# Kernel tuning notes

Hardware: AMD Instinct MI355X
Metric: run time of the kernel (lower is better)

Reference implementation:

```python
import jax, jax.numpy as jnp
import numpy as np

B, H, W, C = 16, 32, 32, 256
N = H * W


def setup_inputs() -> dict:
    key = jax.random.key(0)
    ks = jax.random.split(key, 8)
    x = jax.random.normal(ks[0], (B, H, W, C), dtype=jnp.float32)
    # nn.LazyLinear(C): weight (C, C), bias (C,)
    scale = 1.0 / np.sqrt(C)
    Wq = jax.random.uniform(ks[1], (C, C), jnp.float32, -scale, scale)
    bq = jax.random.uniform(ks[2], (C,), jnp.float32, -scale, scale)
    Wk = jax.random.uniform(ks[3], (C, C), jnp.float32, -scale, scale)
    bk = jax.random.uniform(ks[4], (C,), jnp.float32, -scale, scale)
    Wv = jax.random.uniform(ks[5], (C, C), jnp.float32, -scale, scale)
    bv = jax.random.uniform(ks[6], (C,), jnp.float32, -scale, scale)
    # torch.randn(H, H*W, W)
    Wp = jax.random.normal(ks[7], (H, N, W), dtype=jnp.float32)
    return {"x": x, "Wq": Wq, "bq": bq, "Wk": Wk, "bk": bk,
            "Wv": Wv, "bv": bv, "Wp": Wp}


def reference(x, Wq, bq, Wk, bk, Wv, bv, Wp):
    b, h, w, c = x.shape
    n = h * w
    # Linear projections (torch Linear: x @ W^T + b), flatten spatial dims to N tokens
    q = (jnp.einsum('bhwc,dc->bhwd', x, Wq) + bq).reshape(b, n, c)
    k = (jnp.einsum('bhwc,dc->bhwd', x, Wk) + bk).reshape(b, n, c)
    v = (jnp.einsum('bhwc,dc->bhwd', x, Wv) + bv).reshape(b, n, c)
    # Unscaled attention over the N spatial tokens (no 1/sqrt(C) in the original)
    scores = jnp.einsum('bnc,bmc->bnm', q, k)          # (B, N, N)
    attn = jax.nn.softmax(scores, axis=-1)
    qkv = jnp.einsum('bnm,bmc->bnc', attn, v)           # (B, N, C)
    # z = (qkv^T [B,1,C,N] @ Wp [H,N,W]).transpose(-2,-1) -> (B, H, W, C)
    z = jnp.einsum('bnc,hnw->bhwc', qkv, Wp)
    return z
```

## Files before the change

### kernel.cpp

```cpp
#include <hip/hip_runtime.h>
#include <hip/hip_bf16.h>

#define BB 16
#define NN 1024
#define CC 256

typedef __attribute__((ext_vector_type(8))) short bf16x8;
typedef __attribute__((ext_vector_type(4))) float f32x4;

#define GPTR(p) ((const __attribute__((address_space(1))) void*)(p))
#define LPTR(p) ((__attribute__((address_space(3))) void*)(p))

__device__ __forceinline__ unsigned short f2bf(float f) {
  union { float f; unsigned u; } v; v.f = f;
  unsigned r = v.u + 0x7FFFu + ((v.u >> 16) & 1u);
  return (unsigned short)(r >> 16);
}

__global__ void cast_all(const float* __restrict__ x,
                         const float* __restrict__ Wq, const float* __restrict__ Wk,
                         const float* __restrict__ Wv,
                         const float* __restrict__ bq, const float* __restrict__ bk,
                         const float* __restrict__ bv,
                         unsigned short* __restrict__ xb,
                         unsigned short* __restrict__ wqkvb,
                         float* __restrict__ bqkv) {
  const int NX = BB * NN * CC;
  const int NW = CC * CC;
  int i = blockIdx.x * blockDim.x + threadIdx.x;
  if (i < NX) { xb[i] = f2bf(x[i]); return; }
  int j = i - NX;
  if (j < 3 * NW) {
    const float* w = (j < NW) ? Wq : (j < 2 * NW ? Wk : Wv);
    wqkvb[j] = f2bf(w[j % NW]);
    return;
  }
  int jj = j - 3 * NW;
  if (jj < 3 * CC) {
    const float* bb = (jj < CC) ? bq : (jj < 2 * CC ? bk : bv);
    bqkv[jj] = bb[jj % CC];
  }
}

__global__ __launch_bounds__(256) void wp_transpose(const float* __restrict__ Wp,
                                                    unsigned short* __restrict__ Amat) {
  __shared__ float tile[32][33];
  int h = blockIdx.y;
  int n0 = blockIdx.x * 32;
#pragma unroll
  for (int j = 0; j < 4; j++) {
    int idx = threadIdx.x + j * 256;
    int a = idx >> 5, wc = idx & 31;
    tile[a][wc] = Wp[(size_t)h * (NN * 32) + (size_t)(n0 + a) * 32 + wc];
  }
  __syncthreads();
#pragma unroll
  for (int j = 0; j < 4; j++) {
    int idx = threadIdx.x + j * 256;
    int wc = idx >> 5, a = idx & 31;
    Amat[(size_t)(h * 32 + wc) * NN + n0 + a] = f2bf(tile[a][wc]);
  }
}

template <int BIAS_MODE, int F32OUT>
__global__ __launch_bounds__(256) void gemm_tile(
    const unsigned short* __restrict__ A, int lda, long sA,
    const unsigned short* __restrict__ Bt, int ldb, long sB,
    const float* __restrict__ bias,
    void* __restrict__ Out, int ldo, long sO, int K) {
  __shared__ unsigned short As[2 * 128 * 32];
  __shared__ unsigned short Bs[2 * 64 * 32];
  int b = blockIdx.x;
  int m0 = blockIdx.y * 128;
  int n0 = blockIdx.z * 64;
  int t = threadIdx.x;
  int w = t >> 6, lane = t & 63;
  int wm = (w >> 1) * 64, wn = (w & 1) * 32;
  int r = lane & 15, g = lane >> 4;

  const unsigned short* Ab = A + (long)b * sA;
  const unsigned short* Bb = Bt + (long)b * sB;

  int srow = t >> 2;
  int scol = (t & 3) * 8;

  f32x4 acc[4][2];
#pragma unroll
  for (int i = 0; i < 4; i++)
#pragma unroll
    for (int j = 0; j < 2; j++) acc[i][j] = (f32x4){0.f, 0.f, 0.f, 0.f};

  for (int k0 = 0; k0 < K; k0 += 64) {
    __syncthreads();
#pragma unroll
    for (int kh = 0; kh < 2; kh++) {
#pragma unroll
      for (int jj = 0; jj < 2; jj++) {
        __builtin_amdgcn_global_load_lds(
            GPTR(Ab + (long)(m0 + srow + jj * 64) * lda + k0 + kh * 32 + scol),
            LPTR(&As[kh * 4096 + jj * 2048 + t * 8]), 16, 0, 0);
      }
      __builtin_amdgcn_global_load_lds(
          GPTR(Bb + (long)(n0 + srow) * ldb + k0 + kh * 32 + scol),
          LPTR(&Bs[kh * 2048 + t * 8]), 16, 0, 0);
    }
    __syncthreads();
#pragma unroll
    for (int kh = 0; kh < 2; kh++) {
      bf16x8 af[4], bfr[2];
#pragma unroll
      for (int ti = 0; ti < 4; ti++)
        af[ti] = *(const bf16x8*)&As[kh * 4096 + (wm + ti * 16 + r) * 32 + g * 8];
#pragma unroll
      for (int tj = 0; tj < 2; tj++)
        bfr[tj] = *(const bf16x8*)&Bs[kh * 2048 + (wn + tj * 16 + r) * 32 + g * 8];
#pragma unroll
      for (int ti = 0; ti < 4; ti++)
#pragma unroll
        for (int tj = 0; tj < 2; tj++)
          acc[ti][tj] = __builtin_amdgcn_mfma_f32_16x16x32_bf16(af[ti], bfr[tj], acc[ti][tj], 0, 0, 0);
    }
  }

#pragma unroll
  for (int ti = 0; ti < 4; ti++) {
#pragma unroll
    for (int tj = 0; tj < 2; tj++) {
      int col = n0 + wn + tj * 16 + r;
      float bc = (BIAS_MODE == 1) ? bias[col] : 0.0f;
#pragma unroll
      for (int rr = 0; rr < 4; rr++) {
        int row = m0 + wm + ti * 16 + g * 4 + rr;
        float val = acc[ti][tj][rr] + bc;
        long oidx = (long)b * sO + (long)row * ldo + col;
        if (F32OUT)
          ((float*)Out)[oidx] = val;
        else
          ((unsigned short*)Out)[oidx] = f2bf(val);
      }
    }
  }
}

__global__ __launch_bounds__(256) void gemm_qkv(
    const unsigned short* __restrict__ A,
    const unsigned short* __restrict__ Bt,
    const float* __restrict__ bias,
    unsigned short* __restrict__ Qb, unsigned short* __restrict__ Kb,
    unsigned short* __restrict__ Vtb) {
  __shared__ unsigned short As[2 * 128 * 32];
  __shared__ unsigned short Bs[2 * 64 * 32];
  int b = blockIdx.x;
  int m0 = blockIdx.y * 128;
  int n0 = blockIdx.z * 64;
  int t = threadIdx.x;
  int w = t >> 6, lane = t & 63;
  int wm = (w >> 1) * 64, wn = (w & 1) * 32;
  int r = lane & 15, g = lane >> 4;

  const unsigned short* Ab = A + (long)b * NN * CC;
  int srow = t >> 2;
  int scol = (t & 3) * 8;

  f32x4 acc[4][2];
#pragma unroll
  for (int i = 0; i < 4; i++)
#pragma unroll
    for (int j = 0; j < 2; j++) acc[i][j] = (f32x4){0.f, 0.f, 0.f, 0.f};

  for (int k0 = 0; k0 < CC; k0 += 64) {
    __syncthreads();
#pragma unroll
    for (int kh = 0; kh < 2; kh++) {
#pragma unroll
      for (int jj = 0; jj < 2; jj++) {
        __builtin_amdgcn_global_load_lds(
            GPTR(Ab + (long)(m0 + srow + jj * 64) * CC + k0 + kh * 32 + scol),
            LPTR(&As[kh * 4096 + jj * 2048 + t * 8]), 16, 0, 0);
      }
      __builtin_amdgcn_global_load_lds(
          GPTR(Bt + (long)(n0 + srow) * CC + k0 + kh * 32 + scol),
          LPTR(&Bs[kh * 2048 + t * 8]), 16, 0, 0);
    }
    __syncthreads();
#pragma unroll
    for (int kh = 0; kh < 2; kh++) {
      bf16x8 af[4], bfr[2];
#pragma unroll
      for (int ti = 0; ti < 4; ti++)
        af[ti] = *(const bf16x8*)&As[kh * 4096 + (wm + ti * 16 + r) * 32 + g * 8];
#pragma unroll
      for (int tj = 0; tj < 2; tj++)
        bfr[tj] = *(const bf16x8*)&Bs[kh * 2048 + (wn + tj * 16 + r) * 32 + g * 8];
#pragma unroll
      for (int ti = 0; ti < 4; ti++)
#pragma unroll
        for (int tj = 0; tj < 2; tj++)
          acc[ti][tj] = __builtin_amdgcn_mfma_f32_16x16x32_bf16(af[ti], bfr[tj], acc[ti][tj], 0, 0, 0);
    }
  }

  int seg = n0 >> 8;
#pragma unroll
  for (int ti = 0; ti < 4; ti++) {
#pragma unroll
    for (int tj = 0; tj < 2; tj++) {
      int col = n0 + wn + tj * 16 + r;
      int c = col & 255;
      float bc = bias[col];
#pragma unroll
      for (int rr = 0; rr < 4; rr++) {
        int row = m0 + wm + ti * 16 + g * 4 + rr;
        float val = acc[ti][tj][rr] + bc;
        long base = (long)b * NN * CC;
        if (seg == 0) {
          Qb[base + (long)row * CC + c] = f2bf(val);
        } else if (seg == 1) {
          Kb[base + ((long)(c >> 5) * NN + row) * 32 + (c & 31)] = f2bf(val);
        } else {
          Vtb[base + ((((long)(c >> 4) * 128 + (row >> 3)) * 16 + (c & 15)) * 8 + (row & 7))] = f2bf(val);
        }
      }
    }
  }
}

__global__ __launch_bounds__(512, 4) void attn_fused(
    const unsigned short* __restrict__ Q,
    const unsigned short* __restrict__ Kt,
    const unsigned short* __restrict__ Vt,
    unsigned short* __restrict__ QKVt) {
  __shared__ unsigned short ShBuf[32 * 1024];
  __shared__ float red[4][2][16];
  int b = blockIdx.x;
  int n0 = blockIdx.y * 32;
  int t = threadIdx.x;
  int w = t >> 6, lane = t & 63;
  int rg = w >> 2, ch = w & 3;
  int r = lane & 15, g = lane >> 4;

  const unsigned short* qbase = Q + ((long)b * NN + n0 + rg * 16 + r) * CC + g * 8;
  bf16x8 qf[8];
#pragma unroll
  for (int kk = 0; kk < 8; kk++) qf[kk] = *(const bf16x8*)(qbase + kk * 32);

  f32x4 acc[16];
#pragma unroll
  for (int tt = 0; tt < 16; tt++) acc[tt] = (f32x4){0.f, 0.f, 0.f, 0.f};

  const unsigned short* kslab = Kt + (long)b * NN * CC;
  for (int kk = 0; kk < 8; kk++) {
    __syncthreads();
#pragma unroll
    for (int j = 0; j < 8; j++) {
      __builtin_amdgcn_global_load_lds(
          GPTR(kslab + (long)kk * NN * 32 + j * 4096 + t * 8),
          LPTR(&ShBuf[j * 4096 + t * 8]), 16, 0, 0);
    }
    __syncthreads();
#pragma unroll
    for (int tt = 0; tt < 16; tt++) {
      bf16x8 bv = *(const bf16x8*)&ShBuf[(ch * 256 + tt * 16 + r) * 32 + g * 8];
      acc[tt] = __builtin_amdgcn_mfma_f32_16x16x32_bf16(qf[kk], bv, acc[tt], 0, 0, 0);
    }
  }

  float mrow[4];
#pragma unroll
  for (int rr = 0; rr < 4; rr++) {
    float m = acc[0][rr];
#pragma unroll
    for (int tt = 1; tt < 16; tt++) m = fmaxf(m, acc[tt][rr]);
#pragma unroll
    for (int d = 1; d < 16; d <<= 1) m = fmaxf(m, __shfl_xor(m, d, 64));
    mrow[rr] = m;
  }
  if (r == 0) {
#pragma unroll
    for (int rr = 0; rr < 4; rr++) red[ch][rg][g * 4 + rr] = mrow[rr];
  }
  __syncthreads();
#pragma unroll
  for (int rr = 0; rr < 4; rr++) {
    float m = red[0][rg][g * 4 + rr];
#pragma unroll
    for (int c2 = 1; c2 < 4; c2++) m = fmaxf(m, red[c2][rg][g * 4 + rr]);
    mrow[rr] = m;
  }
  __syncthreads();
  float ssum[4];
#pragma unroll
  for (int rr = 0; rr < 4; rr++) {
    float s = 0.f;
#pragma unroll
    for (int tt = 0; tt < 16; tt++) {
      float e = exp2f((acc[tt][rr] - mrow[rr]) * 1.44269504088896f);
      acc[tt][rr] = e;
      s += e;
    }
#pragma unroll
    for (int d = 1; d < 16; d <<= 1) s += __shfl_xor(s, d, 64);
    ssum[rr] = s;
  }
  if (r == 0) {
#pragma unroll
    for (int rr = 0; rr < 4; rr++) red[ch][rg][g * 4 + rr] = ssum[rr];
  }
  __syncthreads();
#pragma unroll
  for (int rr = 0; rr < 4; rr++) {
    float s = red[0][rg][g * 4 + rr] + red[1][rg][g * 4 + rr] +
              red[2][rg][g * 4 + rr] + red[3][rg][g * 4 + rr];
    float inv = 1.0f / s;
    int prow = rg * 16 + g * 4 + rr;
    int sw = prow & 7;
#pragma unroll
    for (int tt = 0; tt < 16; tt++) {
      int col = ch * 256 + tt * 16 + r;
      int chunk = (col >> 3) ^ sw;
      ShBuf[prow * 1024 + chunk * 8 + (col & 7)] = f2bf(acc[tt][rr] * inv);
    }
  }
  __syncthreads();

  const unsigned short* vbase = Vt + (long)b * NN * CC;
  int cw = w * 32;
  f32x4 o[2][2];
#pragma unroll
  for (int i = 0; i < 2; i++)
#pragma unroll
    for (int j = 0; j < 2; j++) o[i][j] = (f32x4){0.f, 0.f, 0.f, 0.f};

#pragma unroll 2
  for (int m0 = 0; m0 < NN; m0 += 32) {
    bf16x8 ar[2], br[2];
#pragma unroll
    for (int bt = 0; bt < 2; bt++) {
      long vidx = (((long)((cw >> 4) + bt) * 128 + (m0 >> 3) + g) * 16 + r) * 8;
      br[bt] = *(const bf16x8*)(vbase + vidx);
    }
#pragma unroll
    for (int rt = 0; rt < 2; rt++) {
      int prow = rt * 16 + r;
      int chunk = ((m0 >> 3) + g) ^ (prow & 7);
      ar[rt] = *(const bf16x8*)&ShBuf[prow * 1024 + chunk * 8];
    }
#pragma unroll
    for (int rt = 0; rt < 2; rt++)
#pragma unroll
      for (int bt = 0; bt < 2; bt++)
        o[rt][bt] = __builtin_amdgcn_mfma_f32_16x16x32_bf16(ar[rt], br[bt], o[rt][bt], 0, 0, 0);
  }

  unsigned short* obase = QKVt + (long)b * NN * CC;
#pragma unroll
  for (int rt = 0; rt < 2; rt++) {
#pragma unroll
    for (int bt = 0; bt < 2; bt++) {
      int c = cw + bt * 16 + r;
#pragma unroll
      for (int rr = 0; rr < 4; rr++) {
        int n = n0 + rt * 16 + g * 4 + rr;
        obase[(long)c * NN + n] = f2bf(o[rt][bt][rr]);
      }
    }
  }
}

extern "C" void kernel_launch(void* const* d_in, const int* in_sizes, int n_in,
                              void* d_out, int out_size, void* d_ws, size_t ws_size,
                              hipStream_t stream) {
  const float* x  = (const float*)d_in[0];
  const float* Wq = (const float*)d_in[1];
  const float* bq = (const float*)d_in[2];
  const float* Wk = (const float*)d_in[3];
  const float* bk = (const float*)d_in[4];
  const float* Wv = (const float*)d_in[5];
  const float* bv = (const float*)d_in[6];
  const float* Wp = (const float*)d_in[7];
  float* out = (float*)d_out;

  const long BNC = (long)BB * NN * CC;

  char* p = (char*)d_ws;
  unsigned short* xb    = (unsigned short*)p; p += BNC * 2;
  unsigned short* wqkvb = (unsigned short*)p; p += 3L * CC * CC * 2;
  float*          bqkv  = (float*)p;          p += 4096;
  unsigned short* Amat  = (unsigned short*)p; p += (long)NN * NN * 2;
  unsigned short* Qb    = (unsigned short*)p; p += BNC * 2;
  unsigned short* Ktb   = (unsigned short*)p; p += BNC * 2;
  unsigned short* Vtb   = (unsigned short*)p; p += BNC * 2;
  unsigned short* QKVt  = (unsigned short*)p; p += BNC * 2;

  const long TOT = BNC + 3L * CC * CC + 3 * CC;
  cast_all<<<(int)((TOT + 255) / 256), 256, 0, stream>>>(
      x, Wq, Wk, Wv, bq, bk, bv, xb, wqkvb, bqkv);
  wp_transpose<<<dim3(NN / 32, 32), 256, 0, stream>>>(Wp, Amat);

  gemm_qkv<<<dim3(BB, 8, 12), 256, 0, stream>>>(xb, wqkvb, bqkv, Qb, Ktb, Vtb);

  attn_fused<<<dim3(BB, NN / 32), 512, 0, stream>>>(Qb, Ktb, Vtb, QKVt);

  gemm_tile<0, 1><<<dim3(BB, 8, 4), 256, 0, stream>>>(
      Amat, NN, 0L, QKVt, NN, (long)NN * CC, nullptr,
      out, CC, (long)NN * CC, NN);
}
```

Measured before the change: 158.1 us.

## Merge cast and Wp transpose kernels, widen QKV GEMM tile, reorder K loads

Combines the cast kernel and the Wp transpose into a single preprocess launch, which removes one kernel launch. The QKV GEMM now uses 128x128 tiles with a K step of 32, halving the grid and raising per-block reuse at the cost of more accumulator registers. In attention, the first K slab is issued before the Q fragments are loaded, and each subsequent slab load is issued right after the MFMAs on the previous one. This overlaps the first global-to-LDS load with Q loading, but the buffer is still single and barriers remain, so overlap is limited.

```diff
diff --git a/kernel.cpp b/kernel.cpp
--- a/kernel.cpp
+++ b/kernel.cpp
@@ -17,36 +17,41 @@
   return (unsigned short)(r >> 16);
 }
 
-__global__ void cast_all(const float* __restrict__ x,
-                         const float* __restrict__ Wq, const float* __restrict__ Wk,
-                         const float* __restrict__ Wv,
-                         const float* __restrict__ bq, const float* __restrict__ bk,
-                         const float* __restrict__ bv,
-                         unsigned short* __restrict__ xb,
-                         unsigned short* __restrict__ wqkvb,
-                         float* __restrict__ bqkv) {
-  const int NX = BB * NN * CC;
-  const int NW = CC * CC;
-  int i = blockIdx.x * blockDim.x + threadIdx.x;
-  if (i < NX) { xb[i] = f2bf(x[i]); return; }
-  int j = i - NX;
-  if (j < 3 * NW) {
-    const float* w = (j < NW) ? Wq : (j < 2 * NW ? Wk : Wv);
-    wqkvb[j] = f2bf(w[j % NW]);
+#define NCAST 17155
+__global__ __launch_bounds__(256) void preprocess(
+    const float* __restrict__ x,
+    const float* __restrict__ Wq, const float* __restrict__ Wk,
+    const float* __restrict__ Wv,
+    const float* __restrict__ bq, const float* __restrict__ bk,
+    const float* __restrict__ bv,
+    const float* __restrict__ Wp,
+    unsigned short* __restrict__ xb,
+    unsigned short* __restrict__ wqkvb,
+    float* __restrict__ bqkv,
+    unsigned short* __restrict__ Amat) {
+  __shared__ float tile[32][33];
+  int blk = blockIdx.x;
+  if (blk < NCAST) {
+    const int NX = BB * NN * CC;
+    const int NW = CC * CC;
+    int i = blk * 256 + threadIdx.x;
+    if (i < NX) { xb[i] = f2bf(x[i]); return; }
+    int j = i - NX;
+    if (j < 3 * NW) {
+      const float* w = (j < NW) ? Wq : (j < 2 * NW ? Wk : Wv);
+      wqkvb[j] = f2bf(w[j % NW]);
+      return;
+    }
+    int jj = j - 3 * NW;
+    if (jj < 3 * CC) {
+      const float* bb = (jj < CC) ? bq : (jj < 2 * CC ? bk : bv);
+      bqkv[jj] = bb[jj % CC];
+    }
     return;
   }
-  int jj = j - 3 * NW;
-  if (jj < 3 * CC) {
-    const float* bb = (jj < CC) ? bq : (jj < 2 * CC ? bk : bv);
-    bqkv[jj] = bb[jj % CC];
-  }
-}
-
-__global__ __launch_bounds__(256) void wp_transpose(const float* __restrict__ Wp,
-                                                    unsigned short* __restrict__ Amat) {
-  __shared__ float tile[32][33];
-  int h = blockIdx.y;
-  int n0 = blockIdx.x * 32;
+  int wb = blk - NCAST;
+  int h = wb >> 5;
+  int n0 = (wb & 31) * 32;
 #pragma unroll
   for (int j = 0; j < 4; j++) {
     int idx = threadIdx.x + j * 256;
@@ -148,63 +153,57 @@
     const float* __restrict__ bias,
     unsigned short* __restrict__ Qb, unsigned short* __restrict__ Kb,
     unsigned short* __restrict__ Vtb) {
-  __shared__ unsigned short As[2 * 128 * 32];
-  __shared__ unsigned short Bs[2 * 64 * 32];
+  __shared__ unsigned short As[128 * 32];
+  __shared__ unsigned short Bs[128 * 32];
   int b = blockIdx.x;
   int m0 = blockIdx.y * 128;
-  int n0 = blockIdx.z * 64;
+  int n0 = blockIdx.z * 128;
   int t = threadIdx.x;
   int w = t >> 6, lane = t & 63;
-  int wm = (w >> 1) * 64, wn = (w & 1) * 32;
+  int wm = (w >> 1) * 64, wn = (w & 1) * 64;
   int r = lane & 15, g = lane >> 4;
 
   const unsigned short* Ab = A + (long)b * NN * CC;
   int srow = t >> 2;
   int scol = (t & 3) * 8;
 
-  f32x4 acc[4][2];
+  f32x4 acc[4][4];
 #pragma unroll
   for (int i = 0; i < 4; i++)
 #pragma unroll
-    for (int j = 0; j < 2; j++) acc[i][j] = (f32x4){0.f, 0.f, 0.f, 0.f};
-
-  for (int k0 = 0; k0 < CC; k0 += 64) {
+    for (int j = 0; j < 4; j++) acc[i][j] = (f32x4){0.f, 0.f, 0.f, 0.f};
+
+  for (int k0 = 0; k0 < CC; k0 += 32) {
     __syncthreads();
 #pragma unroll
-    for (int kh = 0; kh < 2; kh++) {
-#pragma unroll
-      for (int jj = 0; jj < 2; jj++) {
-        __builtin_amdgcn_global_load_lds(
-            GPTR(Ab + (long)(m0 + srow + jj * 64) * CC + k0 + kh * 32 + scol),
-            LPTR(&As[kh * 4096 + jj * 2048 + t * 8]), 16, 0, 0);
-      }
+    for (int jj = 0; jj < 2; jj++) {
       __builtin_amdgcn_global_load_lds(
-          GPTR(Bt + (long)(n0 + srow) * CC + k0 + kh * 32 + scol),
-          LPTR(&Bs[kh * 2048 + t * 8]), 16, 0, 0);
+          GPTR(Ab + (long)(m0 + srow + jj * 64) * CC + k0 + scol),
+          LPTR(&As[jj * 2048 + t * 8]), 16, 0, 0);
+      __builtin_amdgcn_global_load_lds(
+          GPTR(Bt + (long)(n0 + srow + jj * 64) * CC + k0 + scol),
+          LPTR(&Bs[jj * 2048 + t * 8]), 16, 0, 0);
     }
     __syncthreads();
-#pragma unroll
-    for (int kh = 0; kh < 2; kh++) {
-      bf16x8 af[4], bfr[2];
-#pragma unroll
-      for (int ti = 0; ti < 4; ti++)
-        af[ti] = *(const bf16x8*)&As[kh * 4096 + (wm + ti * 16 + r) * 32 + g * 8];
-#pragma unroll
-      for (int tj = 0; tj < 2; tj++)
-        bfr[tj] = *(const bf16x8*)&Bs[kh * 2048 + (wn + tj * 16 + r) * 32 + g * 8];
-#pragma unroll
-      for (int ti = 0; ti < 4; ti++)
-#pragma unroll
-        for (int tj = 0; tj < 2; tj++)
-          acc[ti][tj] = __builtin_amdgcn_mfma_f32_16x16x32_bf16(af[ti], bfr[tj], acc[ti][tj], 0, 0, 0);
-    }
+    bf16x8 af[4], bfr[4];
+#pragma unroll
+    for (int ti = 0; ti < 4; ti++)
+      af[ti] = *(const bf16x8*)&As[(wm + ti * 16 + r) * 32 + g * 8];
+#pragma unroll
+    for (int tj = 0; tj < 4; tj++)
+      bfr[tj] = *(const bf16x8*)&Bs[(wn + tj * 16 + r) * 32 + g * 8];
+#pragma unroll
+    for (int ti = 0; ti < 4; ti++)
+#pragma unroll
+      for (int tj = 0; tj < 4; tj++)
+        acc[ti][tj] = __builtin_amdgcn_mfma_f32_16x16x32_bf16(af[ti], bfr[tj], acc[ti][tj], 0, 0, 0);
   }
 
   int seg = n0 >> 8;
 #pragma unroll
   for (int ti = 0; ti < 4; ti++) {
 #pragma unroll
-    for (int tj = 0; tj < 2; tj++) {
+    for (int tj = 0; tj < 4; tj++) {
       int col = n0 + wn + tj * 16 + r;
       int c = col & 255;
       float bc = bias[col];
@@ -239,6 +238,13 @@
   int rg = w >> 2, ch = w & 3;
   int r = lane & 15, g = lane >> 4;
 
+  const unsigned short* kslab = Kt + (long)b * NN * CC;
+#pragma unroll
+  for (int j = 0; j < 8; j++) {
+    __builtin_amdgcn_global_load_lds(
+        GPTR(kslab + j * 4096 + t * 8),
+        LPTR(&ShBuf[j * 4096 + t * 8]), 16, 0, 0);
+  }
   const unsigned short* qbase = Q + ((long)b * NN + n0 + rg * 16 + r) * CC + g * 8;
   bf16x8 qf[8];
 #pragma unroll
@@ -248,20 +254,21 @@
 #pragma unroll
   for (int tt = 0; tt < 16; tt++) acc[tt] = (f32x4){0.f, 0.f, 0.f, 0.f};
 
-  const unsigned short* kslab = Kt + (long)b * NN * CC;
   for (int kk = 0; kk < 8; kk++) {
-    __syncthreads();
-#pragma unroll
-    for (int j = 0; j < 8; j++) {
-      __builtin_amdgcn_global_load_lds(
-          GPTR(kslab + (long)kk * NN * 32 + j * 4096 + t * 8),
-          LPTR(&ShBuf[j * 4096 + t * 8]), 16, 0, 0);
-    }
     __syncthreads();
 #pragma unroll
     for (int tt = 0; tt < 16; tt++) {
       bf16x8 bv = *(const bf16x8*)&ShBuf[(ch * 256 + tt * 16 + r) * 32 + g * 8];
       acc[tt] = __builtin_amdgcn_mfma_f32_16x16x32_bf16(qf[kk], bv, acc[tt], 0, 0, 0);
+    }
+    if (kk < 7) {
+      __syncthreads();
+#pragma unroll
+      for (int j = 0; j < 8; j++) {
+        __builtin_amdgcn_global_load_lds(
+            GPTR(kslab + (long)(kk + 1) * NN * 32 + j * 4096 + t * 8),
+            LPTR(&ShBuf[j * 4096 + t * 8]), 16, 0, 0);
+      }
     }
   }
 
@@ -392,12 +399,10 @@
   unsigned short* Vtb   = (unsigned short*)p; p += BNC * 2;
   unsigned short* QKVt  = (unsigned short*)p; p += BNC * 2;
 
-  const long TOT = BNC + 3L * CC * CC + 3 * CC;
-  cast_all<<<(int)((TOT + 255) / 256), 256, 0, stream>>>(
-      x, Wq, Wk, Wv, bq, bk, bv, xb, wqkvb, bqkv);
-  wp_transpose<<<dim3(NN / 32, 32), 256, 0, stream>>>(Wp, Amat);
-
-  gemm_qkv<<<dim3(BB, 8, 12), 256, 0, stream>>>(xb, wqkvb, bqkv, Qb, Ktb, Vtb);
+  preprocess<<<NCAST + 1024, 256, 0, stream>>>(
+      x, Wq, Wk, Wv, bq, bk, bv, Wp, xb, wqkvb, bqkv, Amat);
+
+  gemm_qkv<<<dim3(BB, 8, 6), 256, 0, stream>>>(xb, wqkvb, bqkv, Qb, Ktb, Vtb);
 
   attn_fused<<<dim3(BB, NN / 32), 512, 0, stream>>>(Qb, Ktb, Vtb, QKVt);
 
```

Result: faster. 153.7 us (-2.8%).
